# Kernel tuning notes

Measured on AMD Instinct MI355X. Metric: run time of the kernel, lower is better.

Reference implementation:

```python
import jax, jax.numpy as jnp
import numpy as np

WS = 16          # window_size
N = WS * WS      # tokens per window
H = 8            # num_heads
HD = 64          # head_dim
DIM = 512
EPEG_K = 15
PAD = EPEG_K // 2


def _relative_position_index(ws):
    coords = np.stack(np.meshgrid(np.arange(ws), np.arange(ws), indexing='ij'))  # (2, ws, ws)
    flat = coords.reshape(2, -1)                                                 # (2, N)
    rel = flat[:, :, None] - flat[:, None, :]                                    # (2, N, N)
    rel = rel.transpose(1, 2, 0).astype(np.int64)                                # (N, N, 2)
    rel[..., 0] += ws - 1
    rel[..., 1] += ws - 1
    rel[..., 0] *= 2 * ws - 1
    return rel.sum(-1)                                                           # (N, N)

REL_IDX = jnp.asarray(_relative_position_index(WS), dtype=jnp.int32)


def setup_inputs() -> dict:
    key = jax.random.key(0)
    ks = jax.random.split(key, 8)
    B_ = 128
    x = jax.random.normal(ks[0], (B_, N, DIM), dtype=jnp.float32)
    qkv_w = jax.random.normal(ks[1], (3 * H * HD, DIM), dtype=jnp.float32) * 0.02
    qkv_b = jnp.zeros((3 * H * HD,), dtype=jnp.float32)
    pe_w = jax.random.normal(ks[2], (H, 1, EPEG_K, 1), dtype=jnp.float32) * 0.02  # depthwise (15,1) conv
    pe_b = jnp.zeros((H,), dtype=jnp.float32)
    rpb_table = jax.random.normal(ks[3], ((2 * WS - 1) * (2 * WS - 1), H), dtype=jnp.float32) * 0.02
    proj_w = jax.random.normal(ks[4], (DIM, H * HD), dtype=jnp.float32) * 0.02
    proj_b = jnp.zeros((DIM,), dtype=jnp.float32)
    return {"x": x, "qkv_w": qkv_w, "qkv_b": qkv_b, "pe_w": pe_w, "pe_b": pe_b,
            "rpb_table": rpb_table, "proj_w": proj_w, "proj_b": proj_b}


def reference(x, qkv_w, qkv_b, pe_w, pe_b, rpb_table, proj_w, proj_b):
    B_, n, _ = x.shape
    scale = HD ** -0.5
    qkv = (x @ qkv_w.T + qkv_b).reshape(B_, n, 3, H, HD).transpose(2, 0, 3, 1, 4)  # (3,B_,H,N,hd)
    q, k, v = qkv[0] * scale, qkv[1], qkv[2]
    attn = jnp.einsum('bhnd,bhmd->bhnm', q, k)                                    # (B_,H,N,N)
    # epeg: depthwise conv (k,1) over the score map, per head
    pe = jax.lax.conv_general_dilated(
        attn, pe_w, window_strides=(1, 1), padding=((PAD, PAD), (0, 0)),
        dimension_numbers=('NCHW', 'OIHW', 'NCHW'), feature_group_count=H)
    attn = attn + pe + pe_b[None, :, None, None]
    bias = rpb_table[REL_IDX.reshape(-1)].reshape(n, n, H).transpose(2, 0, 1)     # (H,N,N)
    attn = jax.nn.softmax(attn + bias[None], axis=-1)
    out = jnp.einsum('bhnm,bhmd->bnhd', attn, v).reshape(B_, n, H * HD)
    return out @ proj_w.T + proj_b
```

## Files before the change

### kernel.cpp

```cpp
#include <hip/hip_runtime.h>


typedef unsigned short u16;
typedef unsigned int u32;
typedef __attribute__((ext_vector_type(8))) short short8;
typedef __attribute__((ext_vector_type(4))) float f32x4;

__device__ __forceinline__ u16 f2bf(float f) {
  union { float f; u32 u; } v; v.f = f;
  return (u16)((v.u + 0x7FFFu + ((v.u >> 16) & 1u)) >> 16);
}
__device__ __forceinline__ float bf2f(u16 s) {
  union { u32 u; float f; } v; v.u = ((u32)s) << 16;
  return v.f;
}
__device__ __forceinline__ u32 cvtpk(float lo, float hi) {
  u32 r;
  asm("v_cvt_pk_bf16_f32 %0, %1, %2" : "=v"(r) : "v"(lo), "v"(hi));
  return r;
}

__device__ __forceinline__ void gl2lds16(const u16* g, u16* l) {
  __builtin_amdgcn_global_load_lds((const __attribute__((address_space(1))) void*)g,
                                   (__attribute__((address_space(3))) void*)l, 16, 0, 0);
}

__device__ __forceinline__ int fragaddr(int frag, int lane) {
  return (frag * 64 + (lane ^ (frag & 7))) * 8;
}

__global__ __launch_bounds__(256) void cvt_all(
    const float* __restrict__ x, const float* __restrict__ w1f,
    const float* __restrict__ w2f, u16* __restrict__ xo,
    u16* __restrict__ w1o, u16* __restrict__ w2o) {
  const int NX = 4194304, NW1 = 196608, NW2 = 65536;
  int i = blockIdx.x * 256 + threadIdx.x;
  const float* src; u16* dst; int j;
  if (i < NX)                  { src = x;   dst = xo;  j = i; }
  else if (i < NX + NW1)       { src = w1f; dst = w1o; j = i - NX; }
  else if (i < NX + NW1 + NW2) { src = w2f; dst = w2o; j = i - NX - NW1; }
  else return;
  float4 f = ((const float4*)src)[j];
  uint2 o;
  o.x = (u32)f2bf(f.x) | ((u32)f2bf(f.y) << 16);
  o.y = (u32)f2bf(f.z) | ((u32)f2bf(f.w) << 16);
  ((uint2*)dst)[j] = o;
}

__device__ __forceinline__ void gemm256_core(
    const u16* __restrict__ A, const u16* __restrict__ B,
    int m0, int n0, u16* lds, f32x4 acc[8][4]) {
  const int NT = 8;
  int tid = threadIdx.x, wave = tid >> 6, lane = tid & 63;
  int wm = wave >> 2, wn = wave & 3;

  int ch0 = tid, ch1 = tid + 512;
  int row0 = ch0 >> 2, row1 = ch1 >> 2;
  int cg0 = (ch0 & 3) ^ (row0 & 3) ^ ((row0 >> 2) & 3);
  int cg1 = (ch1 & 3) ^ (row1 & 3) ^ ((row1 >> 2) & 3);
  const u16* Ag0 = A + (size_t)(m0 + row0) * 512 + cg0 * 8;
  const u16* Ag1 = A + (size_t)(m0 + row1) * 512 + cg1 * 8;
  const u16* Bg0 = B + (size_t)(n0 + row0) * 512 + cg0 * 8;
  const u16* Bg1 = B + (size_t)(n0 + row1) * 512 + cg1 * 8;
  int ldsu0 = wave * 64 * 8;
  int ldsu1 = (512 + wave * 64) * 8;

  int frag_off = (lane & 15) * 32 +
                 (((lane >> 4) ^ (lane & 3) ^ ((lane >> 2) & 3)) << 3);
  int abase = wm * 4096 + frag_off;
  int bbase = 8192 + wn * 2048 + frag_off;

#define STAGE(h)                                                             \
  do {                                                                       \
    if ((h) < NT * 4) {                                                      \
      int T_ = (h) >> 2, kh_ = ((h) >> 1) & 1, isB_ = (h) & 1;               \
      int ko_ = T_ * 64 + kh_ * 32;                                          \
      u16* d_ = lds + (T_ & 1) * 32768 + kh_ * 16384 + isB_ * 8192;          \
      gl2lds16((isB_ ? Bg0 : Ag0) + ko_, d_ + ldsu0);                        \
      gl2lds16((isB_ ? Bg1 : Ag1) + ko_, d_ + ldsu1);                        \
    }                                                                        \
  } while (0)

#define LDA(dst, mf, kh, p)                                                  \
  dst = *(const short8*)(lds + (p) * 32768 + (kh) * 16384 + abase + (mf) * 512)
#define LDB(dst, nf, kh, p)                                                  \
  dst = *(const short8*)(lds + (p) * 32768 + (kh) * 16384 + bbase + (nf) * 512)

#define MM16(M0)                                                                                   \
  __builtin_amdgcn_s_setprio(1);                                                                   \
  acc[(M0)+0][0] = __builtin_amdgcn_mfma_f32_16x16x32_bf16(a0, b0, acc[(M0)+0][0], 0, 0, 0);       \
  acc[(M0)+0][1] = __builtin_amdgcn_mfma_f32_16x16x32_bf16(a0, b1, acc[(M0)+0][1], 0, 0, 0);       \
  acc[(M0)+0][2] = __builtin_amdgcn_mfma_f32_16x16x32_bf16(a0, b2, acc[(M0)+0][2], 0, 0, 0);       \
  acc[(M0)+0][3] = __builtin_amdgcn_mfma_f32_16x16x32_bf16(a0, b3, acc[(M0)+0][3], 0, 0, 0);       \
  acc[(M0)+1][0] = __builtin_amdgcn_mfma_f32_16x16x32_bf16(a1, b0, acc[(M0)+1][0], 0, 0, 0);       \
  acc[(M0)+1][1] = __builtin_amdgcn_mfma_f32_16x16x32_bf16(a1, b1, acc[(M0)+1][1], 0, 0, 0);       \
  acc[(M0)+1][2] = __builtin_amdgcn_mfma_f32_16x16x32_bf16(a1, b2, acc[(M0)+1][2], 0, 0, 0);       \
  acc[(M0)+1][3] = __builtin_amdgcn_mfma_f32_16x16x32_bf16(a1, b3, acc[(M0)+1][3], 0, 0, 0);       \
  acc[(M0)+2][0] = __builtin_amdgcn_mfma_f32_16x16x32_bf16(a2, b0, acc[(M0)+2][0], 0, 0, 0);       \
  acc[(M0)+2][1] = __builtin_amdgcn_mfma_f32_16x16x32_bf16(a2, b1, acc[(M0)+2][1], 0, 0, 0);       \
  acc[(M0)+2][2] = __builtin_amdgcn_mfma_f32_16x16x32_bf16(a2, b2, acc[(M0)+2][2], 0, 0, 0);       \
  acc[(M0)+2][3] = __builtin_amdgcn_mfma_f32_16x16x32_bf16(a2, b3, acc[(M0)+2][3], 0, 0, 0);       \
  acc[(M0)+3][0] = __builtin_amdgcn_mfma_f32_16x16x32_bf16(a3, b0, acc[(M0)+3][0], 0, 0, 0);       \
  acc[(M0)+3][1] = __builtin_amdgcn_mfma_f32_16x16x32_bf16(a3, b1, acc[(M0)+3][1], 0, 0, 0);       \
  acc[(M0)+3][2] = __builtin_amdgcn_mfma_f32_16x16x32_bf16(a3, b2, acc[(M0)+3][2], 0, 0, 0);       \
  acc[(M0)+3][3] = __builtin_amdgcn_mfma_f32_16x16x32_bf16(a3, b3, acc[(M0)+3][3], 0, 0, 0);       \
  __builtin_amdgcn_s_setprio(0)

  STAGE(0); STAGE(1); STAGE(2); STAGE(3); STAGE(4);
  asm volatile("s_waitcnt vmcnt(6)" ::: "memory");
  __builtin_amdgcn_s_barrier();

#pragma unroll 1
  for (int kt = 0; kt < NT; ++kt) {
    int p = kt & 1;
    int hb = kt * 4 + 5;
    short8 a0, a1, a2, a3, b0, b1, b2, b3;
    LDA(a0, 0, 0, p); LDA(a1, 1, 0, p); LDA(a2, 2, 0, p); LDA(a3, 3, 0, p);
    LDB(b0, 0, 0, p); LDB(b1, 1, 0, p); LDB(b2, 2, 0, p); LDB(b3, 3, 0, p);
    STAGE(hb);
    __builtin_amdgcn_s_barrier();
    asm volatile("s_waitcnt lgkmcnt(0)" ::: "memory");
    MM16(0);
    __builtin_amdgcn_s_barrier();
    LDA(a0, 4, 0, p); LDA(a1, 5, 0, p); LDA(a2, 6, 0, p); LDA(a3, 7, 0, p);
    STAGE(hb + 1);
    __builtin_amdgcn_s_barrier();
    asm volatile("s_waitcnt lgkmcnt(0)" ::: "memory");
    MM16(4);
    if (kt == NT - 1) asm volatile("s_waitcnt vmcnt(0)" ::: "memory");
    else              asm volatile("s_waitcnt vmcnt(6)" ::: "memory");
    __builtin_amdgcn_s_barrier();
    LDA(a0, 0, 1, p); LDA(a1, 1, 1, p); LDA(a2, 2, 1, p); LDA(a3, 3, 1, p);
    LDB(b0, 0, 1, p); LDB(b1, 1, 1, p); LDB(b2, 2, 1, p); LDB(b3, 3, 1, p);
    STAGE(hb + 2);
    __builtin_amdgcn_s_barrier();
    asm volatile("s_waitcnt lgkmcnt(0)" ::: "memory");
    MM16(0);
    __builtin_amdgcn_s_barrier();
    LDA(a0, 4, 1, p); LDA(a1, 5, 1, p); LDA(a2, 6, 1, p); LDA(a3, 7, 1, p);
    STAGE(hb + 3);
    __builtin_amdgcn_s_barrier();
    asm volatile("s_waitcnt lgkmcnt(0)" ::: "memory");
    MM16(4);
    if (kt == NT - 2)     asm volatile("s_waitcnt vmcnt(4)" ::: "memory");
    else if (kt < NT - 2) asm volatile("s_waitcnt vmcnt(6)" ::: "memory");
    __builtin_amdgcn_s_barrier();
  }
#undef STAGE
#undef LDA
#undef LDB
#undef MM16
}

__global__ __launch_bounds__(512, 2) void gemm_qkv256(
    const u16* __restrict__ A, const u16* __restrict__ B,
    const float* __restrict__ qkvb, u16* __restrict__ qb,
    u16* __restrict__ kb, u16* __restrict__ vb) {
  __shared__ __align__(16) u16 lds[65536];
  f32x4 acc[8][4];
#pragma unroll
  for (int a = 0; a < 8; ++a)
#pragma unroll
    for (int c = 0; c < 4; ++c) acc[a][c] = (f32x4){0.f, 0.f, 0.f, 0.f};
  int bid = blockIdx.x;
  int wg = (bid & 7) * 96 + (bid >> 3);
  int m0 = (wg / 6) * 256, n0 = (wg % 6) * 256;
  gemm256_core(A, B, m0, n0, lds, acc);

  int tid = threadIdx.x, wave = tid >> 6, lane = tid & 63;
  int wm = wave >> 2, wn = wave & 3;
  int cx = lane & 15, g = lane >> 4;

  __syncthreads();
#pragma unroll
  for (int nf = 0; nf < 4; ++nf) {
    int cb = wn * 64 + nf * 16;
    int cgl = n0 + cb + cx;
    float bv = qkvb[cgl];
    float sc = ((cgl >> 9) == 0) ? 0.125f : 1.f;
#pragma unroll
    for (int mf = 0; mf < 8; ++mf) {
#pragma unroll
      for (int i = 0; i < 4; ++i) {
        int r = wm * 128 + mf * 16 + g * 4 + i;
        int c = cb + cx;
        int c16 = (c >> 3) ^ (((r >> 2) & 3) << 1);
        lds[r * 256 + c16 * 8 + (c & 7)] = f2bf((acc[mf][nf][i] + bv) * sc);
      }
    }
  }
  __syncthreads();

  int b = m0 >> 8;
#pragma unroll
  for (int j = 0; j < 16; ++j) {
    const int hg = j >> 2;
    int gcol = n0 + hg * 64;
    int which = gcol >> 9;
    int h = (gcol >> 6) & 7;
    u16* dst = (which == 0 ? qb : (which == 1 ? kb : vb)) +
               (size_t)(b * 8 + h) * 16384;
    int n = (j & 3) * 64 + (tid >> 3);
    int dc = tid & 7;
    int c16 = (hg * 8 + dc) ^ (((n >> 2) & 3) << 1);
    uint4 val = *(const uint4*)(lds + n * 256 + c16 * 8);
    *(uint4*)(dst + n * 64 + dc * 8) = val;
  }
}

__global__ __launch_bounds__(512, 2) void gemm_proj256(
    const u16* __restrict__ A, const u16* __restrict__ B,
    const float* __restrict__ pb, float* __restrict__ out) {
  __shared__ __align__(16) u16 lds[65536];
  f32x4 acc[8][4];
#pragma unroll
  for (int a = 0; a < 8; ++a)
#pragma unroll
    for (int c = 0; c < 4; ++c) acc[a][c] = (f32x4){0.f, 0.f, 0.f, 0.f};
  int bid = blockIdx.x;
  int wg = (bid & 7) * 32 + (bid >> 3);
  int m0 = (wg >> 1) * 256, n0 = (wg & 1) * 256;
  gemm256_core(A, B, m0, n0, lds, acc);
  int tid = threadIdx.x, wave = tid >> 6, lane = tid & 63;
  int wm = wave >> 2, wn = wave & 3;
  float bv[4];
#pragma unroll
  for (int nf = 0; nf < 4; ++nf)
    bv[nf] = pb[n0 + wn * 64 + nf * 16 + (lane & 15)];
#pragma unroll
  for (int mf = 0; mf < 8; ++mf) {
#pragma unroll
    for (int i = 0; i < 4; ++i) {
      int r = m0 + wm * 128 + mf * 16 + (lane >> 4) * 4 + i;
#pragma unroll
      for (int nf = 0; nf < 4; ++nf) {
        int c = n0 + wn * 64 + nf * 16 + (lane & 15);
        out[(size_t)r * 512 + c] = acc[mf][nf][i] + bv[nf];
      }
    }
  }
}

__global__ __launch_bounds__(256) void qconv(u16* __restrict__ qb,
                                             const float* __restrict__ pe_w) {
  __shared__ __align__(16) u16 Ql[256 * 72];
  __shared__ float w[15];
  int bh = blockIdx.x, h = bh & 7, tid = threadIdx.x;
  const uint4* src = (const uint4*)(qb + (size_t)bh * 16384);
#pragma unroll
  for (int it = 0; it < 8; ++it) {
    int idx = tid + it * 256;
    int row = idx >> 3, c = (idx & 7) * 8;
    *(uint4*)(Ql + row * 72 + c) = src[idx];
  }
  if (tid < 15) w[tid] = pe_w[h * 15 + tid] + (tid == 7 ? 1.f : 0.f);
  __syncthreads();
  int dg = (tid & 15) * 4, nb4 = tid >> 4;
  uint2* dst = (uint2*)(qb + (size_t)bh * 16384);
#pragma unroll
  for (int i = 0; i < 16; ++i) {
    int n = nb4 + i * 16;
    float a0 = 0.f, a1 = 0.f, a2 = 0.f, a3 = 0.f;
#pragma unroll
    for (int t = 0; t < 15; ++t) {
      int nn = n + t - 7;
      if (nn < 0 || nn > 255) continue;
      uint2 rv = *(const uint2*)(Ql + nn * 72 + dg);
      float wt = w[t];
      a0 += wt * bf2f(rv.x & 0xffff); a1 += wt * bf2f(rv.x >> 16);
      a2 += wt * bf2f(rv.y & 0xffff); a3 += wt * bf2f(rv.y >> 16);
    }
    uint2 pv;
    pv.x = (u32)f2bf(a0) | ((u32)f2bf(a1) << 16);
    pv.y = (u32)f2bf(a2) | ((u32)f2bf(a3) << 16);
    dst[(n * 64 + dg) >> 2] = pv;
  }
}

__global__ __launch_bounds__(512, 2) void attn_win(
    const u16* __restrict__ qb, const u16* __restrict__ kb,
    const u16* __restrict__ vb, const float* __restrict__ pe_b,
    const float* __restrict__ rpb, u16* __restrict__ attnout) {
  __shared__ __align__(16) u16 KfPs[21504];
  __shared__ __align__(16) u16 Vf[16384];
  __shared__ float biasl[961];

  int bh = blockIdx.x, b = bh >> 3, h = bh & 7;
  int tid = threadIdx.x, wave = tid >> 6, lane = tid & 63;
  int cx = lane & 15, g = lane >> 4;

  const uint4* kg = (const uint4*)(kb + (size_t)bh * 16384);
  const uint4* vg = (const uint4*)(vb + (size_t)bh * 16384);
  const u16* qgb = qb + (size_t)bh * 16384;

  short8 qfr0a = *(const short8*)(qgb + (0 * 128 + wave * 16 + cx) * 64 + g * 8);
  short8 qfr0b = *(const short8*)(qgb + (0 * 128 + wave * 16 + cx) * 64 + 32 + g * 8);
  short8 qfr1a = *(const short8*)(qgb + (1 * 128 + wave * 16 + cx) * 64 + g * 8);
  short8 qfr1b = *(const short8*)(qgb + (1 * 128 + wave * 16 + cx) * 64 + 32 + g * 8);

  uint4 kreg[4];
#pragma unroll
  for (int it = 0; it < 4; ++it) kreg[it] = kg[tid + it * 512];

  u16* Vtmp = KfPs;
#pragma unroll
  for (int it = 0; it < 4; ++it) {
    int idx = tid + it * 512;
    uint4 v = vg[idx];
    int row = idx >> 3, c8 = (idx & 7) * 8;
    *(uint2*)(Vtmp + row * 68 + c8)     = make_uint2(v.x, v.y);
    *(uint2*)(Vtmp + row * 68 + c8 + 4) = make_uint2(v.z, v.w);
  }
  {
    float peb = pe_b[h];
    for (int i = tid; i < 961; i += 512) biasl[i] = rpb[i * 8 + h] + peb;
  }
  __syncthreads();

#pragma unroll
  for (int it = 0; it < 4; ++it) {
    int o = tid + it * 512;
    int frag = o >> 6, lanep = o & 63;
    int d = (frag >> 3) * 16 + (lanep & 15);
    int mb = (frag & 7) * 32 + (lanep >> 4) * 8;
    uint4 pk;
    pk.x = (u32)Vtmp[(mb + 0) * 68 + d] | ((u32)Vtmp[(mb + 1) * 68 + d] << 16);
    pk.y = (u32)Vtmp[(mb + 2) * 68 + d] | ((u32)Vtmp[(mb + 3) * 68 + d] << 16);
    pk.z = (u32)Vtmp[(mb + 4) * 68 + d] | ((u32)Vtmp[(mb + 5) * 68 + d] << 16);
    pk.w = (u32)Vtmp[(mb + 6) * 68 + d] | ((u32)Vtmp[(mb + 7) * 68 + d] << 16);
    *(uint4*)(Vf + (frag * 64 + (lanep ^ (frag & 7))) * 8) = pk;
  }
  __syncthreads();

  u16* Kf = KfPs;
#pragma unroll
  for (int it = 0; it < 4; ++it) {
    int idx = tid + it * 512;
    int n = idx >> 3, k8 = idx & 7;
    int frag = (n >> 4) * 2 + (k8 >> 2);
    int lanep = (n & 15) + 16 * (k8 & 3);
    *(uint4*)(Kf + (frag * 64 + (lanep ^ (frag & 7))) * 8) = kreg[it];
  }
  __syncthreads();

  u16* Psw = KfPs + 16384 + wave * 640;

#pragma unroll
  for (int it2 = 0; it2 < 2; ++it2) {
    short8 qf0 = it2 ? qfr1a : qfr0a;
    short8 qf1 = it2 ? qfr1b : qfr0b;
    int qbase = it2 * 128 + wave * 16;

    float m_run = -1e30f, l_run = 0.f;
    f32x4 oacc[4];
#pragma unroll
    for (int dt = 0; dt < 4; ++dt) oacc[dt] = (f32x4){0.f, 0.f, 0.f, 0.f};

#pragma unroll
    for (int c = 0; c < 2; ++c) {
      f32x4 acc[8];
#pragma unroll
      for (int mt = 0; mt < 8; ++mt) acc[mt] = (f32x4){0.f, 0.f, 0.f, 0.f};
      __builtin_amdgcn_s_setprio(1);
#pragma unroll
      for (int mt = 0; mt < 8; ++mt) {
        int fr = (c * 8 + mt) * 2;
        short8 k0 = *(const short8*)(Kf + fragaddr(fr, lane));
        short8 k1 = *(const short8*)(Kf + fragaddr(fr + 1, lane));
        acc[mt] = __builtin_amdgcn_mfma_f32_16x16x32_bf16(k0, qf0, acc[mt], 0, 0, 0);
        acc[mt] = __builtin_amdgcn_mfma_f32_16x16x32_bf16(k1, qf1, acc[mt], 0, 0, 0);
      }
      __builtin_amdgcn_s_setprio(0);

      int nb = (it2 * 8 + wave - c * 8 + 15) * 31 + cx - g * 4 + 15;
#pragma unroll
      for (int mt = 0; mt < 8; ++mt) {
        const float* bp = biasl + (nb - 31 * mt);
        acc[mt][0] += bp[0];  acc[mt][1] += bp[-1];
        acc[mt][2] += bp[-2]; acc[mt][3] += bp[-3];
      }

      float mx = fmaxf(fmaxf(acc[0][0], acc[0][1]), fmaxf(acc[0][2], acc[0][3]));
#pragma unroll
      for (int mt = 1; mt < 8; ++mt)
        mx = fmaxf(mx, fmaxf(fmaxf(acc[mt][0], acc[mt][1]),
                             fmaxf(acc[mt][2], acc[mt][3])));
      mx = fmaxf(mx, __shfl_xor(mx, 16));
      mx = fmaxf(mx, __shfl_xor(mx, 32));
      float mnew = fmaxf(m_run, mx);
      float al = __expf(m_run - mnew);
      float s = 0.f;
#pragma unroll
      for (int mt = 0; mt < 8; ++mt)
#pragma unroll
        for (int i = 0; i < 4; ++i) {
          float e = __expf(acc[mt][i] - mnew);
          acc[mt][i] = e; s += e;
        }
      s += __shfl_xor(s, 16);
      s += __shfl_xor(s, 32);
      l_run = l_run * al + s;
      m_run = mnew;

      float alr[4];
#pragma unroll
      for (int i = 0; i < 4; ++i) alr[i] = __shfl(al, g * 4 + i);
#pragma unroll
      for (int dt = 0; dt < 4; ++dt)
#pragma unroll
        for (int i = 0; i < 4; ++i) oacc[dt][i] *= alr[i];

#pragma unroll
      for (int kk = 0; kk < 4; ++kk) {
        u32 w0 = cvtpk(acc[2 * kk][0], acc[2 * kk][1]);
        u32 w1 = cvtpk(acc[2 * kk][2], acc[2 * kk][3]);
        u32 w2 = cvtpk(acc[2 * kk + 1][0], acc[2 * kk + 1][1]);
        u32 w3 = cvtpk(acc[2 * kk + 1][2], acc[2 * kk + 1][3]);
        *(uint2*)(Psw + cx * 40 + g * 4)      = make_uint2(w0, w1);
        *(uint2*)(Psw + cx * 40 + 16 + g * 4) = make_uint2(w2, w3);
        short8 pa = *(const short8*)(Psw + cx * 40 + g * 8);
        __builtin_amdgcn_s_setprio(1);
#pragma unroll
        for (int dt = 0; dt < 4; ++dt) {
          short8 vf = *(const short8*)(Vf + fragaddr(dt * 8 + c * 4 + kk, lane));
          oacc[dt] = __builtin_amdgcn_mfma_f32_16x16x32_bf16(pa, vf, oacc[dt], 0, 0, 0);
        }
        __builtin_amdgcn_s_setprio(0);
      }
    }

    float inv = 1.f / l_run;
    float inv4[4];
#pragma unroll
    for (int i = 0; i < 4; ++i) inv4[i] = __shfl(inv, g * 4 + i);
#pragma unroll
    for (int dt = 0; dt < 4; ++dt)
#pragma unroll
      for (int i = 0; i < 4; ++i)
        attnout[((size_t)b * 256 + qbase + g * 4 + i) * 512 + h * 64 + dt * 16 + cx]
            = f2bf(oacc[dt][i] * inv4[i]);
  }
}

extern "C" void kernel_launch(void* const* d_in, const int* in_sizes, int n_in,
                              void* d_out, int out_size, void* d_ws, size_t ws_size,
                              hipStream_t stream) {
  const float* x      = (const float*)d_in[0];
  const float* qkv_w  = (const float*)d_in[1];
  const float* qkv_b  = (const float*)d_in[2];
  const float* pe_w   = (const float*)d_in[3];
  const float* pe_b   = (const float*)d_in[4];
  const float* rpb    = (const float*)d_in[5];
  const float* proj_w = (const float*)d_in[6];
  const float* proj_b = (const float*)d_in[7];
  float* out = (float*)d_out;
  char* ws = (char*)d_ws;

  size_t off = 0;
  u16* xbf = (u16*)(ws + off); off += (size_t)16777216 * 2;
  u16* w1  = (u16*)(ws + off); off += (size_t)786432 * 2;
  u16* w2  = (u16*)(ws + off); off += (size_t)262144 * 2;
  u16* qb  = (u16*)(ws + off); off += (size_t)16777216 * 2;
  u16* kb  = (u16*)(ws + off); off += (size_t)16777216 * 2;
  u16* vb  = (u16*)(ws + off); off += (size_t)16777216 * 2;

  hipLaunchKernelGGL(cvt_all, dim3(17408), dim3(256), 0, stream,
                     x, qkv_w, proj_w, xbf, w1, w2);
  hipLaunchKernelGGL(gemm_qkv256, dim3(768), dim3(512), 0, stream,
                     xbf, w1, qkv_b, qb, kb, vb);
  hipLaunchKernelGGL(qconv, dim3(1024), dim3(256), 0, stream, qb, pe_w);
  hipLaunchKernelGGL(attn_win, dim3(1024), dim3(512), 0, stream,
                     qb, kb, vb, pe_b, rpb, xbf);
  hipLaunchKernelGGL(gemm_proj256, dim3(256), dim3(512), 0, stream,
                     xbf, w2, proj_b, out);
}
```

Before: 294.0 us.

## Swap MFMA operands to get transposed accumulators and vectorize epilogue stores

Swaps the A/B operands of the MFMA calls in the GEMM core and in the attention PV product, so each lane's accumulator holds four consecutive columns instead of four rows. The QKV epilogue can then write packed bf16 directly to global memory, skipping the LDS staging round trip and its two barriers. The proj epilogue writes float4 and the attention output writes uint2. In attention the per-row shuffles of the rescale factor and inverse sum become unnecessary. The risk is that the direct global stores are less coalesced than the previous LDS-staged 16-byte stores.

```diff
diff --git a/kernel.cpp b/kernel.cpp
--- a/kernel.cpp
+++ b/kernel.cpp
@@ -88,22 +88,22 @@
 
 #define MM16(M0)                                                                                   \
   __builtin_amdgcn_s_setprio(1);                                                                   \
-  acc[(M0)+0][0] = __builtin_amdgcn_mfma_f32_16x16x32_bf16(a0, b0, acc[(M0)+0][0], 0, 0, 0);       \
-  acc[(M0)+0][1] = __builtin_amdgcn_mfma_f32_16x16x32_bf16(a0, b1, acc[(M0)+0][1], 0, 0, 0);       \
-  acc[(M0)+0][2] = __builtin_amdgcn_mfma_f32_16x16x32_bf16(a0, b2, acc[(M0)+0][2], 0, 0, 0);       \
-  acc[(M0)+0][3] = __builtin_amdgcn_mfma_f32_16x16x32_bf16(a0, b3, acc[(M0)+0][3], 0, 0, 0);       \
-  acc[(M0)+1][0] = __builtin_amdgcn_mfma_f32_16x16x32_bf16(a1, b0, acc[(M0)+1][0], 0, 0, 0);       \
-  acc[(M0)+1][1] = __builtin_amdgcn_mfma_f32_16x16x32_bf16(a1, b1, acc[(M0)+1][1], 0, 0, 0);       \
-  acc[(M0)+1][2] = __builtin_amdgcn_mfma_f32_16x16x32_bf16(a1, b2, acc[(M0)+1][2], 0, 0, 0);       \
-  acc[(M0)+1][3] = __builtin_amdgcn_mfma_f32_16x16x32_bf16(a1, b3, acc[(M0)+1][3], 0, 0, 0);       \
-  acc[(M0)+2][0] = __builtin_amdgcn_mfma_f32_16x16x32_bf16(a2, b0, acc[(M0)+2][0], 0, 0, 0);       \
-  acc[(M0)+2][1] = __builtin_amdgcn_mfma_f32_16x16x32_bf16(a2, b1, acc[(M0)+2][1], 0, 0, 0);       \
-  acc[(M0)+2][2] = __builtin_amdgcn_mfma_f32_16x16x32_bf16(a2, b2, acc[(M0)+2][2], 0, 0, 0);       \
-  acc[(M0)+2][3] = __builtin_amdgcn_mfma_f32_16x16x32_bf16(a2, b3, acc[(M0)+2][3], 0, 0, 0);       \
-  acc[(M0)+3][0] = __builtin_amdgcn_mfma_f32_16x16x32_bf16(a3, b0, acc[(M0)+3][0], 0, 0, 0);       \
-  acc[(M0)+3][1] = __builtin_amdgcn_mfma_f32_16x16x32_bf16(a3, b1, acc[(M0)+3][1], 0, 0, 0);       \
-  acc[(M0)+3][2] = __builtin_amdgcn_mfma_f32_16x16x32_bf16(a3, b2, acc[(M0)+3][2], 0, 0, 0);       \
-  acc[(M0)+3][3] = __builtin_amdgcn_mfma_f32_16x16x32_bf16(a3, b3, acc[(M0)+3][3], 0, 0, 0);       \
+  acc[(M0)+0][0] = __builtin_amdgcn_mfma_f32_16x16x32_bf16(b0, a0, acc[(M0)+0][0], 0, 0, 0);       \
+  acc[(M0)+0][1] = __builtin_amdgcn_mfma_f32_16x16x32_bf16(b1, a0, acc[(M0)+0][1], 0, 0, 0);       \
+  acc[(M0)+0][2] = __builtin_amdgcn_mfma_f32_16x16x32_bf16(b2, a0, acc[(M0)+0][2], 0, 0, 0);       \
+  acc[(M0)+0][3] = __builtin_amdgcn_mfma_f32_16x16x32_bf16(b3, a0, acc[(M0)+0][3], 0, 0, 0);       \
+  acc[(M0)+1][0] = __builtin_amdgcn_mfma_f32_16x16x32_bf16(b0, a1, acc[(M0)+1][0], 0, 0, 0);       \
+  acc[(M0)+1][1] = __builtin_amdgcn_mfma_f32_16x16x32_bf16(b1, a1, acc[(M0)+1][1], 0, 0, 0);       \
+  acc[(M0)+1][2] = __builtin_amdgcn_mfma_f32_16x16x32_bf16(b2, a1, acc[(M0)+1][2], 0, 0, 0);       \
+  acc[(M0)+1][3] = __builtin_amdgcn_mfma_f32_16x16x32_bf16(b3, a1, acc[(M0)+1][3], 0, 0, 0);       \
+  acc[(M0)+2][0] = __builtin_amdgcn_mfma_f32_16x16x32_bf16(b0, a2, acc[(M0)+2][0], 0, 0, 0);       \
+  acc[(M0)+2][1] = __builtin_amdgcn_mfma_f32_16x16x32_bf16(b1, a2, acc[(M0)+2][1], 0, 0, 0);       \
+  acc[(M0)+2][2] = __builtin_amdgcn_mfma_f32_16x16x32_bf16(b2, a2, acc[(M0)+2][2], 0, 0, 0);       \
+  acc[(M0)+2][3] = __builtin_amdgcn_mfma_f32_16x16x32_bf16(b3, a2, acc[(M0)+2][3], 0, 0, 0);       \
+  acc[(M0)+3][0] = __builtin_amdgcn_mfma_f32_16x16x32_bf16(b0, a3, acc[(M0)+3][0], 0, 0, 0);       \
+  acc[(M0)+3][1] = __builtin_amdgcn_mfma_f32_16x16x32_bf16(b1, a3, acc[(M0)+3][1], 0, 0, 0);       \
+  acc[(M0)+3][2] = __builtin_amdgcn_mfma_f32_16x16x32_bf16(b2, a3, acc[(M0)+3][2], 0, 0, 0);       \
+  acc[(M0)+3][3] = __builtin_amdgcn_mfma_f32_16x16x32_bf16(b3, a3, acc[(M0)+3][3], 0, 0, 0);       \
   __builtin_amdgcn_s_setprio(0)
 
   STAGE(0); STAGE(1); STAGE(2); STAGE(3); STAGE(4);
@@ -170,41 +170,31 @@
   int tid = threadIdx.x, wave = tid >> 6, lane = tid & 63;
   int wm = wave >> 2, wn = wave & 3;
   int cx = lane & 15, g = lane >> 4;
-
-  __syncthreads();
+  int b = m0 >> 8;
+
+  u16* dstn[4]; float scn[4]; float4 bsn[4];
 #pragma unroll
   for (int nf = 0; nf < 4; ++nf) {
-    int cb = wn * 64 + nf * 16;
-    int cgl = n0 + cb + cx;
-    float bv = qkvb[cgl];
-    float sc = ((cgl >> 9) == 0) ? 0.125f : 1.f;
-#pragma unroll
-    for (int mf = 0; mf < 8; ++mf) {
-#pragma unroll
-      for (int i = 0; i < 4; ++i) {
-        int r = wm * 128 + mf * 16 + g * 4 + i;
-        int c = cb + cx;
-        int c16 = (c >> 3) ^ (((r >> 2) & 3) << 1);
-        lds[r * 256 + c16 * 8 + (c & 7)] = f2bf((acc[mf][nf][i] + bv) * sc);
-      }
+    int c0 = n0 + wn * 64 + nf * 16 + g * 4;
+    int which = c0 >> 9, cc = c0 & 511, h = cc >> 6, d0 = cc & 63;
+    float sc = (which == 0) ? 0.125f : 1.f;
+    float4 bv = *(const float4*)(qkvb + c0);
+    scn[nf] = sc;
+    bsn[nf] = make_float4(bv.x * sc, bv.y * sc, bv.z * sc, bv.w * sc);
+    dstn[nf] = (which == 0 ? qb : (which == 1 ? kb : vb)) +
+               (size_t)(b * 8 + h) * 16384 + d0;
+  }
+  int ntok = wm * 128 + cx;
+#pragma unroll
+  for (int mf = 0; mf < 8; ++mf) {
+    int off = (ntok + mf * 16) * 64;
+#pragma unroll
+    for (int nf = 0; nf < 4; ++nf) {
+      f32x4 v = acc[mf][nf];
+      u32 w0 = cvtpk(v[0] * scn[nf] + bsn[nf].x, v[1] * scn[nf] + bsn[nf].y);
+      u32 w1 = cvtpk(v[2] * scn[nf] + bsn[nf].z, v[3] * scn[nf] + bsn[nf].w);
+      *(uint2*)(dstn[nf] + off) = make_uint2(w0, w1);
     }
-  }
-  __syncthreads();
-
-  int b = m0 >> 8;
-#pragma unroll
-  for (int j = 0; j < 16; ++j) {
-    const int hg = j >> 2;
-    int gcol = n0 + hg * 64;
-    int which = gcol >> 9;
-    int h = (gcol >> 6) & 7;
-    u16* dst = (which == 0 ? qb : (which == 1 ? kb : vb)) +
-               (size_t)(b * 8 + h) * 16384;
-    int n = (j & 3) * 64 + (tid >> 3);
-    int dc = tid & 7;
-    int c16 = (hg * 8 + dc) ^ (((n >> 2) & 3) << 1);
-    uint4 val = *(const uint4*)(lds + n * 256 + c16 * 8);
-    *(uint4*)(dst + n * 64 + dc * 8) = val;
   }
 }
 
@@ -221,22 +211,24 @@
   int wg = (bid & 7) * 32 + (bid >> 3);
   int m0 = (wg >> 1) * 256, n0 = (wg & 1) * 256;
   gemm256_core(A, B, m0, n0, lds, acc);
+
   int tid = threadIdx.x, wave = tid >> 6, lane = tid & 63;
   int wm = wave >> 2, wn = wave & 3;
-  float bv[4];
-#pragma unroll
-  for (int nf = 0; nf < 4; ++nf)
-    bv[nf] = pb[n0 + wn * 64 + nf * 16 + (lane & 15)];
+  int cx = lane & 15, g = lane >> 4;
+  int cb = n0 + wn * 64 + g * 4;
+  float4 bv[4];
+#pragma unroll
+  for (int nf = 0; nf < 4; ++nf) bv[nf] = *(const float4*)(pb + cb + nf * 16);
+  int r0 = m0 + wm * 128 + cx;
 #pragma unroll
   for (int mf = 0; mf < 8; ++mf) {
-#pragma unroll
-    for (int i = 0; i < 4; ++i) {
-      int r = m0 + wm * 128 + mf * 16 + (lane >> 4) * 4 + i;
-#pragma unroll
-      for (int nf = 0; nf < 4; ++nf) {
-        int c = n0 + wn * 64 + nf * 16 + (lane & 15);
-        out[(size_t)r * 512 + c] = acc[mf][nf][i] + bv[nf];
-      }
+    size_t rb = (size_t)(r0 + mf * 16) * 512;
+#pragma unroll
+    for (int nf = 0; nf < 4; ++nf) {
+      f32x4 v = acc[mf][nf];
+      float4 o = make_float4(v[0] + bv[nf].x, v[1] + bv[nf].y,
+                             v[2] + bv[nf].z, v[3] + bv[nf].w);
+      *(float4*)(out + rb + cb + nf * 16) = o;
     }
   }
 }
@@ -402,13 +394,10 @@
       l_run = l_run * al + s;
       m_run = mnew;
 
-      float alr[4];
-#pragma unroll
-      for (int i = 0; i < 4; ++i) alr[i] = __shfl(al, g * 4 + i);
 #pragma unroll
       for (int dt = 0; dt < 4; ++dt)
 #pragma unroll
-        for (int i = 0; i < 4; ++i) oacc[dt][i] *= alr[i];
+        for (int i = 0; i < 4; ++i) oacc[dt][i] *= al;
 
 #pragma unroll
       for (int kk = 0; kk < 4; ++kk) {
@@ -423,22 +412,20 @@
 #pragma unroll
         for (int dt = 0; dt < 4; ++dt) {
           short8 vf = *(const short8*)(Vf + fragaddr(dt * 8 + c * 4 + kk, lane));
-          oacc[dt] = __builtin_amdgcn_mfma_f32_16x16x32_bf16(pa, vf, oacc[dt], 0, 0, 0);
+          oacc[dt] = __builtin_amdgcn_mfma_f32_16x16x32_bf16(vf, pa, oacc[dt], 0, 0, 0);
         }
         __builtin_amdgcn_s_setprio(0);
       }
     }
 
     float inv = 1.f / l_run;
-    float inv4[4];
-#pragma unroll
-    for (int i = 0; i < 4; ++i) inv4[i] = __shfl(inv, g * 4 + i);
-#pragma unroll
-    for (int dt = 0; dt < 4; ++dt)
-#pragma unroll
-      for (int i = 0; i < 4; ++i)
-        attnout[((size_t)b * 256 + qbase + g * 4 + i) * 512 + h * 64 + dt * 16 + cx]
-            = f2bf(oacc[dt][i] * inv4[i]);
+    u16* ao = attnout + ((size_t)b * 256 + qbase + cx) * 512 + h * 64;
+#pragma unroll
+    for (int dt = 0; dt < 4; ++dt) {
+      u32 w0 = cvtpk(oacc[dt][0] * inv, oacc[dt][1] * inv);
+      u32 w1 = cvtpk(oacc[dt][2] * inv, oacc[dt][3] * inv);
+      *(uint2*)(ao + dt * 16 + g * 4) = make_uint2(w0, w1);
+    }
   }
 }
 
```

Result: slower. 315.8 us (+7.4%).
